# Performance work log

Measured on AMD Instinct MI355X. Metric: run time of the kernel, lower is better.

The kernel has to match this reference:

```python
import jax, jax.numpy as jnp
import numpy as np

EPS_DIAG = 1e-3  # matches torch.eye(len(A)) * 0.001


def _sqrtm_psd(M):
    # Symmetric PSD matrix square root via eigendecomposition.
    # Equivalent to scipy.linalg.sqrtm(...).real for SPD inputs.
    M = 0.5 * (M + M.T)
    w, v = jnp.linalg.eigh(M)
    w = jnp.clip(w, 0.0)
    return (v * jnp.sqrt(w)) @ v.T


def setup_inputs() -> dict:
    key = jax.random.key(0)
    k1, k2 = jax.random.split(key)
    N, D = 4096, 2048
    z_a = jax.random.normal(k1, (N, D), dtype=jnp.float32)
    z_b = jax.random.normal(k2, (N, D), dtype=jnp.float32)
    return {"z_a": z_a, "z_b": z_b}


def reference(z_a, z_b):
    # norm=True branch: per-feature standardization; torch std uses ddof=1
    n = z_a.shape[0]
    z_a = (z_a - z_a.mean(axis=0)) / (z_a.std(axis=0, ddof=1))
    z_b = (z_b - z_b.mean(axis=0)) / (z_b.std(axis=0, ddof=1))
    A = z_a.T @ z_a  # [D, D]
    B = z_b.T @ z_b  # [D, D]
    D = A.shape[0]
    eps = jnp.eye(D, dtype=A.dtype) * EPS_DIAG
    A = A + eps
    B = B + eps
    B12 = _sqrtm_psd(B)
    C = _sqrtm_psd(B12 @ A @ B12)
    return jnp.trace(A + B - 2.0 * C)
```

## Files before the change

kernel.cpp:

```cpp
#include <hip/hip_runtime.h>
#include <math.h>

typedef unsigned short u16;
typedef unsigned int u32;

#define D_DIM 2048
#define N_ROWS 4096
#define EPS_DIAG 1e-3f
#define NS_ITERS 16

typedef __attribute__((ext_vector_type(8))) short bf16x8;
typedef __attribute__((ext_vector_type(4))) float f32x4;

__device__ __forceinline__ u16 f2bf(float f) {
  u32 u = __float_as_uint(f);
  u += 0x7fffu + ((u >> 16) & 1u);
  return (u16)(u >> 16);
}
__device__ __forceinline__ float bf2f(u16 h) {
  return __uint_as_float(((u32)h) << 16);
}

#define GLD16(g, l)                                        \
  __builtin_amdgcn_global_load_lds(                        \
      (const __attribute__((address_space(1))) void*)(g),  \
      (__attribute__((address_space(3))) void*)(l), 16, 0, 0)



__device__ __forceinline__ void swz256(int id, int& bi, int& bj) {
  int s = id & 7;
  int j = id >> 3;
  bj = s * 2 + (j & 1);
  bi = j >> 1;
}


__global__ __launch_bounds__(256)
void k_colstats2(const float* __restrict__ za, const float* __restrict__ zb,
                 float* __restrict__ stat) {
  const float* z = blockIdx.z ? zb : za;
  float* sum_ = stat + blockIdx.z * 2 * D_DIM;
  float* ssq_ = sum_ + D_DIM;
  const int c = blockIdx.x * 256 + threadIdx.x;
  const int r0 = blockIdx.y * (N_ROWS / 16);
  float s = 0.f, q = 0.f;
#pragma unroll 8
  for (int r = 0; r < N_ROWS / 16; ++r) {
    float v = z[(size_t)(r0 + r) * D_DIM + c];
    s += v;
    q += v * v;
  }
  atomicAdd(&sum_[c], s);
  atomicAdd(&ssq_[c], q);
}

__global__ __launch_bounds__(256)
void k_finalize_stats(float* stat) {
  const int t = blockIdx.x * 256 + threadIdx.x;
  const int g = t >> 11;
  const int c = t & (D_DIM - 1);
  float* base = stat + g * 2 * D_DIM;
  float s = base[c];
  float q = base[D_DIM + c];
  float mean = s * (1.0f / N_ROWS);
  float var = (q - (float)N_ROWS * mean * mean) * (1.0f / (N_ROWS - 1));
  var = fmaxf(var, 1e-30f);
  base[c] = mean;
  base[D_DIM + c] = 1.0f / sqrtf(var);
}


__global__ __launch_bounds__(256)
void k_zsplit_t2(const float* __restrict__ za, const float* __restrict__ zb,
                 const float* __restrict__ stat, u16* __restrict__ Zh0,
                 u16* __restrict__ Zl0, u16* __restrict__ Zh1,
                 u16* __restrict__ Zl1) {
  __shared__ float T[64 * 72];
  const float* z = blockIdx.z ? zb : za;
  const float* mean = stat + blockIdx.z * 2 * D_DIM;
  const float* rstd = mean + D_DIM;
  u16* Zth = blockIdx.z ? Zh1 : Zh0;
  u16* Ztl = blockIdx.z ? Zl1 : Zl0;
  const int t = threadIdx.x;
  const int r0 = blockIdx.x * 64;
  const int c0 = blockIdx.y * 64;
#pragma unroll
  for (int p = 0; p < 4; ++p) {
    int row = p * 16 + (t >> 4);
    int c4 = t & 15;
    float4 v = *(const float4*)(z + (size_t)(r0 + row) * D_DIM + c0 + c4 * 4);
    *(float4*)&T[row * 72 + c4 * 4] = v;
  }
  __syncthreads();
  const int c = c0 + (t >> 2);
  const float m = mean[c];
  const float r = rstd[c];
  const int cc = t >> 2;
#pragma unroll
  for (int g = 0; g < 2; ++g) {
    int rbase = g * 32 + (t & 3) * 8;
    u16 hs[8], ls[8];
#pragma unroll
    for (int i = 0; i < 8; ++i) {
      float x = (T[(rbase + i) * 72 + cc] - m) * r;
      hs[i] = f2bf(x);
      ls[i] = f2bf(x - bf2f(hs[i]));
    }
    uint4 ph, pl;
    ph.x = (u32)hs[0] | ((u32)hs[1] << 16);
    ph.y = (u32)hs[2] | ((u32)hs[3] << 16);
    ph.z = (u32)hs[4] | ((u32)hs[5] << 16);
    ph.w = (u32)hs[6] | ((u32)hs[7] << 16);
    pl.x = (u32)ls[0] | ((u32)ls[1] << 16);
    pl.y = (u32)ls[2] | ((u32)ls[3] << 16);
    pl.z = (u32)ls[4] | ((u32)ls[5] << 16);
    pl.w = (u32)ls[6] | ((u32)ls[7] << 16);
    int n = r0 + rbase;
    int slot = ((n >> 3) & 7) ^ (c & 7);
    size_t o = (size_t)c * N_ROWS + (size_t)((n & ~63) | (slot << 3));
    *(uint4*)(Zth + o) = ph;
    *(uint4*)(Ztl + o) = pl;
  }
}

#define FINVC 1
#define FTRACE 4
#define FCOL 8
#define FROW 16

__device__ __forceinline__ void nn_body(
    u16* lds, const u16* __restrict__ Xh, const u16* __restrict__ Xl,
    const u16* __restrict__ Wh, const u16* __restrict__ Wl,
    u16* __restrict__ Crh, u16* __restrict__ Crl, u16* __restrict__ Cch,
    u16* __restrict__ Ccl, float* __restrict__ scal, int K, float diag,
    float pmul, int flags, int tidx, int bi, int bj) {
  const int tid = threadIdx.x;
  const int lane = tid & 63;
  const int w = tid >> 6;
  const int I = bi * 128;
  const int J = bj * 128;

  size_t xro[4], wro[4];
  int lbase[4];
#pragma unroll
  for (int p = 0; p < 4; ++p) {
    int rl = w * 32 + p * 8;
    xro[p] = (size_t)(I + rl + (lane >> 3)) * K + (lane & 7) * 8;
    wro[p] = (size_t)(J + rl + (lane >> 3)) * K + (lane & 7) * 8;
    lbase[p] = rl * 64;
  }

  f32x4 acc[2][8];
#pragma unroll
  for (int i = 0; i < 2; ++i)
#pragma unroll
    for (int j = 0; j < 8; ++j) acc[i][j] = (f32x4){0.f, 0.f, 0.f, 0.f};

#define NN_STAGE(k1, buf)                                         \
  {                                                               \
    _Pragma("unroll") for (int p = 0; p < 4; ++p) {               \
      GLD16(Xh + xro[p] + (k1), &lds[(buf) + lbase[p]]);          \
      GLD16(Xl + xro[p] + (k1), &lds[(buf) + 8192 + lbase[p]]);   \
      GLD16(Wh + wro[p] + (k1), &lds[(buf) + 16384 + lbase[p]]);  \
      GLD16(Wl + wro[p] + (k1), &lds[(buf) + 24576 + lbase[p]]);  \
    }                                                             \
  }

#define NN_COMPUTE(CUR)                                                   \
  {                                                                       \
    _Pragma("unroll") for (int ks = 0; ks < 2; ++ks) {                    \
      bf16x8 fxh[2], fxl[2];                                              \
      _Pragma("unroll") for (int i = 0; i < 2; ++i) {                     \
        int m = w * 32 + i * 16 + (lane & 15);                            \
        int sl = m * 64 + (((ks * 4 + (lane >> 4)) ^ (m & 7)) << 3);      \
        fxh[i] = *(const bf16x8*)&lds[(CUR) + sl];                        \
        fxl[i] = *(const bf16x8*)&lds[(CUR) + 8192 + sl];                 \
      }                                                                   \
      _Pragma("unroll") for (int jb = 0; jb < 2; ++jb) {                  \
        bf16x8 fwh[4], fwl[4];                                            \
        _Pragma("unroll") for (int jj = 0; jj < 4; ++jj) {                \
          int n = (jb * 4 + jj) * 16 + (lane & 15);                       \
          int sl = n * 64 + (((ks * 4 + (lane >> 4)) ^ (n & 7)) << 3);    \
          fwh[jj] = *(const bf16x8*)&lds[(CUR) + 16384 + sl];             \
          fwl[jj] = *(const bf16x8*)&lds[(CUR) + 24576 + sl];             \
        }                                                                 \
        _Pragma("unroll") for (int i = 0; i < 2; ++i)                     \
          _Pragma("unroll") for (int jj = 0; jj < 4; ++jj) {              \
            acc[i][jb * 4 + jj] = __builtin_amdgcn_mfma_f32_16x16x32_bf16(\
                fxh[i], fwh[jj], acc[i][jb * 4 + jj], 0, 0, 0);           \
            acc[i][jb * 4 + jj] = __builtin_amdgcn_mfma_f32_16x16x32_bf16(\
                fxh[i], fwl[jj], acc[i][jb * 4 + jj], 0, 0, 0);           \
            acc[i][jb * 4 + jj] = __builtin_amdgcn_mfma_f32_16x16x32_bf16(\
                fxl[i], fwh[jj], acc[i][jb * 4 + jj], 0, 0, 0);           \
          }                                                               \
      }                                                                   \
    }                                                                     \
  }

  const int nk = K >> 6;
  NN_STAGE(0, 0);
  for (int k = 0; k < nk; ++k) {
    const int cur = (k & 1) * 32768;
    const int nxt = 32768 - cur;
    __builtin_amdgcn_s_barrier();
    __builtin_amdgcn_sched_barrier(0);
    if (k + 1 < nk) {
      NN_STAGE((k + 1) * 64, nxt);
      __builtin_amdgcn_sched_barrier(0);
      asm volatile("s_waitcnt vmcnt(16)" ::: "memory");
    } else {
      asm volatile("s_waitcnt vmcnt(0)" ::: "memory");
    }
    __builtin_amdgcn_s_barrier();
    __builtin_amdgcn_sched_barrier(0);
    NN_COMPUTE(cur);
  }
  __syncthreads();
#undef NN_COMPUTE
#undef NN_STAGE

  const int qd = lane >> 4;
  const int nl = lane & 15;
  float pm = pmul;
  if (flags & FINVC) pm = pmul / scal[5];

#define NN_VAL(i, j, r, out)                           \
  {                                                    \
    int gi_ = I + w * 32 + (i)*16 + qd * 4 + (r);      \
    int gj_ = J + (j)*16 + nl;                         \
    out = pm * acc[i][j][r];                           \
    if (gi_ == gj_) out += diag;                       \
  }

  if (flags & FTRACE) {
    float ts = 0.f;
#pragma unroll
    for (int i = 0; i < 2; ++i)
#pragma unroll
      for (int j = 0; j < 8; ++j)
#pragma unroll
        for (int r = 0; r < 4; ++r) {
          int gi = I + w * 32 + i * 16 + qd * 4 + r;
          int gj = J + j * 16 + nl;
          if (gi == gj) {
            float v;
            NN_VAL(i, j, r, v);
            ts += v;
          }
        }
#pragma unroll
    for (int o = 32; o > 0; o >>= 1) ts += __shfl_down(ts, o, 64);
    float* red = (float*)lds;
    if (lane == 0) red[w] = ts;
    __syncthreads();
    if (tid == 0) atomicAdd(&scal[tidx], red[0] + red[1] + red[2] + red[3]);
    __syncthreads();
  }

  const int wbp = w * 4352;
  for (int half = 0; half < 2; ++half) {
#pragma unroll
    for (int i = 0; i < 2; ++i)
#pragma unroll
      for (int j = 0; j < 8; ++j)
#pragma unroll
        for (int r = 0; r < 4; ++r) {
          float v;
          NN_VAL(i, j, r, v);
          u16 hv = f2bf(v);
          u16 sv = half ? f2bf(v - bf2f(hv)) : hv;
          lds[wbp + (i * 16 + qd * 4 + r) * 136 + j * 16 + nl] = sv;
        }
    __syncthreads();
    if (flags & FROW) {
      u16* dst = half ? Crl : Crh;
#pragma unroll
      for (int p2 = 0; p2 < 8; ++p2) {
        int rr = lane >> 1;
        int ch = (lane & 1) + p2 * 2;
        bf16x8 vv = *(const bf16x8*)&lds[wbp + rr * 136 + ch * 8];
        int gi = I + w * 32 + rr;
        int slot = (ch & 7) ^ (gi & 7);
        size_t o = (size_t)gi * D_DIM + J + ((ch >> 3) << 6) + (slot << 3);
        *(bf16x8*)(dst + o) = vv;
      }
    }
    if (flags & FCOL) {
      u16* dst = half ? Ccl : Cch;
#pragma unroll
      for (int jj = 0; jj < 8; ++jj) {
        int cmaj = J + jj * 16 + (lane >> 2);
        int run = (lane & 3) * 8;
        int m = I + w * 32 + run;
        u16 tp[8];
#pragma unroll
        for (int r2 = 0; r2 < 8; ++r2) tp[r2] = lds[wbp + (run + r2) * 136 +
                                                    jj * 16 + (lane >> 2)];
        uint4 pk;
        pk.x = (u32)tp[0] | ((u32)tp[1] << 16);
        pk.y = (u32)tp[2] | ((u32)tp[3] << 16);
        pk.z = (u32)tp[4] | ((u32)tp[5] << 16);
        pk.w = (u32)tp[6] | ((u32)tp[7] << 16);
        int slot = ((m >> 3) & 7) ^ (cmaj & 7);
        size_t o = (size_t)cmaj * D_DIM + (m & ~63) + (slot << 3);
        *(uint4*)(dst + o) = pk;
      }
    }
    __syncthreads();
  }
#undef NN_VAL
}

__global__ __launch_bounds__(256)
void k_nn(const u16* Xh, const u16* Xl, const u16* Wh, const u16* Wl, u16* Crh,
          u16* Crl, u16* Cch, u16* Ccl, float* scal, int K, float diag,
          float pmul, int flags, int tidx) {
  __shared__ u16 lds[65536];
  int bi, bj;
  swz256(blockIdx.x + (blockIdx.y << 4), bi, bj);
  nn_body(lds, Xh, Xl, Wh, Wl, Crh, Crl, Cch, Ccl, scal, K, diag, pmul, flags,
          tidx, bi, bj);
}

__global__ __launch_bounds__(256)
void k_nn_tri2(const u16* Xh0, const u16* Xl0, u16* Ch0, u16* Cl0,
               const u16* Xh1, const u16* Xl1, u16* Ch1, u16* Cl1,
               float* scal) {
  __shared__ u16 lds[65536];
  int x = blockIdx.x;
  int f5 = (x & 7) * 34 + (x >> 3);
  int g = (f5 >= 136) ? 1 : 0;
  int f = f5 - g * 136;
  int bi = (int)((sqrtf(8.f * (float)f + 1.f) - 1.f) * 0.5f);
  while (bi * (bi + 1) / 2 > f) --bi;
  while ((bi + 1) * (bi + 2) / 2 <= f) ++bi;
  int bj = f - bi * (bi + 1) / 2;
  if (g)
    nn_body(lds, Xh1, Xl1, Xh1, Xl1, Ch1, Cl1, Ch1, Cl1, scal, N_ROWS,
            EPS_DIAG, 1.0f, FROW | FCOL | FTRACE, 2, bi, bj);
  else
    nn_body(lds, Xh0, Xl0, Xh0, Xl0, Ch0, Cl0, Ch0, Cl0, scal, N_ROWS,
            EPS_DIAG, 1.0f, FROW | FCOL | FTRACE, 1, bi, bj);
}

struct NN2Args {
  const u16 *xh0, *xl0, *wh0, *wl0;
  u16 *crh0, *crl0, *cch0, *ccl0;
  const u16 *xh1, *xl1, *wh1, *wl1;
  u16 *crh1, *crl1, *cch1, *ccl1;
  float pm0, pm1;
};

__global__ __launch_bounds__(256)
void k_nn2(NN2Args a, float* scal) {
  __shared__ u16 lds[65536];
  int bi, bj;
  swz256(blockIdx.x + (blockIdx.y << 4), bi, bj);
  if (blockIdx.z == 0)
    nn_body(lds, a.xh0, a.xl0, a.wh0, a.wl0, a.crh0, a.crl0, a.cch0, a.ccl0,
            scal, D_DIM, 0.f, a.pm0, FROW | FCOL, 0, bi, bj);
  else
    nn_body(lds, a.xh1, a.xl1, a.wh1, a.wl1, a.crh1, a.crl1, a.cch1, a.ccl1,
            scal, D_DIM, 0.f, a.pm1, FROW | FCOL, 0, bi, bj);
}


__global__ __launch_bounds__(256)
void k_pones2(float* __restrict__ va, float* __restrict__ vb,
              float* __restrict__ snA, float* __restrict__ snB) {
  int t = blockIdx.x * 256 + threadIdx.x;
  if (t < D_DIM)
    va[t] = 1.0f;
  else
    vb[t - D_DIM] = 1.0f;
  if (t == 0) {
    snA[0] = 1.0f;
    snB[0] = 1.0f;
  }
}

__global__ __launch_bounds__(256)
void k_gemv2(const u16* __restrict__ Ah, const u16* __restrict__ Bh,
             const float* viA, float* voA, const float* viB, float* voB,
             const float* snA, const float* snB, u32* smA, u32* smB) {
  const int zc = blockIdx.y;
  const u16* Mh = zc ? Bh : Ah;
  const float* vin = zc ? viB : viA;
  float* vout = zc ? voB : voA;
  const float* snorm = zc ? snB : snA;
  u32* smax = zc ? smB : smA;
  __shared__ float vs[D_DIM];
  float inv = 1.0f / snorm[0];
  for (int i = threadIdx.x; i < D_DIM; i += 256) vs[i] = vin[i] * inv;
  __syncthreads();
  int row = blockIdx.x * 4 + (threadIdx.x >> 6);
  int lane = threadIdx.x & 63;
  const u16* r = Mh + (size_t)row * D_DIM;
  float s = 0.f;
  for (int c0 = lane * 8; c0 < D_DIM; c0 += 512) {
    int k0 = (c0 & ~63) | ((((c0 >> 3) & 7) ^ (row & 7)) << 3);
    uint4 p = *(const uint4*)(r + c0);
    u32 w4[4] = {p.x, p.y, p.z, p.w};
#pragma unroll
    for (int q = 0; q < 4; ++q) {
      s += bf2f((u16)(w4[q] & 0xffff)) * vs[k0 + 2 * q];
      s += bf2f((u16)(w4[q] >> 16)) * vs[k0 + 2 * q + 1];
    }
  }
#pragma unroll
  for (int o = 32; o > 0; o >>= 1) s += __shfl_down(s, o, 64);
  if (lane == 0) {
    vout[row] = s;
    atomicMax(smax, __float_as_uint(fabsf(s)));
  }
}

__global__ void k_setc(float* scal) {
  scal[5] = 1.1f * scal[11] * scal[21];
}

__global__ __launch_bounds__(256)
void k_t1(const u16* __restrict__ Mrh, const u16* __restrict__ Mrl,
          const u16* __restrict__ Mth, const u16* __restrict__ Mtl,
          const float* __restrict__ scal, u16* __restrict__ Trh,
          u16* __restrict__ Trl, u16* __restrict__ Tth, u16* __restrict__ Ttl) {
  size_t t = (size_t)blockIdx.x * 256 + threadIdx.x;
  float invc = 1.0f / scal[5];
  size_t e = t * 4;
  int i = (int)(e >> 11);
  int u0 = (int)(e & (D_DIM - 1));
  int jb = (u0 & ~63) | ((((u0 >> 3) & 7) ^ (i & 7)) << 3) | (u0 & 7);
#pragma unroll
  for (int pass = 0; pass < 2; ++pass) {
    const u16* sh = pass ? Mth : Mrh;
    const u16* sl = pass ? Mtl : Mrl;
    u16* dh = pass ? Tth : Trh;
    u16* dl = pass ? Ttl : Trl;
    uint2 hv = ((const uint2*)sh)[t];
    uint2 lv = ((const uint2*)sl)[t];
    u16 hs[4] = {(u16)(hv.x & 0xffff), (u16)(hv.x >> 16), (u16)(hv.y & 0xffff),
                 (u16)(hv.y >> 16)};
    u16 ls[4] = {(u16)(lv.x & 0xffff), (u16)(lv.x >> 16), (u16)(lv.y & 0xffff),
                 (u16)(lv.y >> 16)};
    u16 th[4], tl[4];
#pragma unroll
    for (int c = 0; c < 4; ++c) {
      float m = bf2f(hs[c]) + bf2f(ls[c]);
      float tv = ((i == jb + c) ? 3.0f : 0.0f) - m * invc;
      th[c] = f2bf(tv);
      tl[c] = f2bf(tv - bf2f(th[c]));
    }
    ((uint2*)dh)[t] = make_uint2((u32)th[0] | ((u32)th[1] << 16),
                                 (u32)th[2] | ((u32)th[3] << 16));
    ((uint2*)dl)[t] = make_uint2((u32)tl[0] | ((u32)tl[1] << 16),
                                 (u32)tl[2] | ((u32)tl[3] << 16));
  }
}

__global__ __launch_bounds__(256)
void k_trdot(const u16* __restrict__ Ah, const u16* __restrict__ Al,
             const u16* __restrict__ Bh, const u16* __restrict__ Bl,
             double* __restrict__ acc) {
  size_t t = (size_t)blockIdx.x * 256 + threadIdx.x;
  uint2 ah = ((const uint2*)Ah)[t], al = ((const uint2*)Al)[t];
  uint2 bh = ((const uint2*)Bh)[t], bl = ((const uint2*)Bl)[t];
  float s = 0.f;
  u32 ha[4] = {ah.x & 0xffffu, ah.x >> 16, ah.y & 0xffffu, ah.y >> 16};
  u32 la[4] = {al.x & 0xffffu, al.x >> 16, al.y & 0xffffu, al.y >> 16};
  u32 hb[4] = {bh.x & 0xffffu, bh.x >> 16, bh.y & 0xffffu, bh.y >> 16};
  u32 lb[4] = {bl.x & 0xffffu, bl.x >> 16, bl.y & 0xffffu, bl.y >> 16};
#pragma unroll
  for (int c = 0; c < 4; ++c)
    s += (bf2f((u16)ha[c]) + bf2f((u16)la[c])) *
         (bf2f((u16)hb[c]) + bf2f((u16)lb[c]));
#pragma unroll
  for (int o = 32; o > 0; o >>= 1) s += __shfl_down(s, o, 64);
  __shared__ float red[4];
  if ((threadIdx.x & 63) == 0) red[threadIdx.x >> 6] = s;
  __syncthreads();
  if (threadIdx.x == 0)
    atomicAdd(acc, (double)(red[0] + red[1] + red[2] + red[3]));
}

__global__ void k_final2(const float* __restrict__ scal,
                         const double* __restrict__ dot,
                         float* __restrict__ out) {
  out[0] = scal[1] + scal[2] - sqrtf(scal[5]) * (float)dot[0];
}


__global__ __launch_bounds__(256)
void k_zsplit(const float* __restrict__ z, const float* __restrict__ mean,
              const float* __restrict__ rstd, u16* __restrict__ zh,
              u16* __restrict__ zl) {
  size_t t = (size_t)blockIdx.x * 256 + threadIdx.x;
  int ci = (int)(t & 511);
  float4 v = ((const float4*)z)[t];
  float4 m = ((const float4*)mean)[ci];
  float4 r = ((const float4*)rstd)[ci];
  float x[4] = {(v.x - m.x) * r.x, (v.y - m.y) * r.y, (v.z - m.z) * r.z,
                (v.w - m.w) * r.w};
  u16 h[4], l[4];
#pragma unroll
  for (int i = 0; i < 4; ++i) {
    h[i] = f2bf(x[i]);
    l[i] = f2bf(x[i] - bf2f(h[i]));
  }
  ((uint2*)zh)[t] = make_uint2((u32)h[0] | ((u32)h[1] << 16),
                               (u32)h[2] | ((u32)h[3] << 16));
  ((uint2*)zl)[t] = make_uint2((u32)l[0] | ((u32)l[1] << 16),
                               (u32)l[2] | ((u32)l[3] << 16));
}

__global__ __launch_bounds__(256)
void k_gram_mm(const u16* __restrict__ zh, const u16* __restrict__ zl,
               u16* __restrict__ Oh, u16* __restrict__ Ol) {
  __shared__ u16 lds[24576];
  const int tid = threadIdx.x;
  const int lane = tid & 63;
  const int w = tid >> 6;
  const int I = blockIdx.y * 128;
  const int J = blockIdx.x * 64;
  const int kp = tid >> 4;
  const int nc = tid & 15;
  const int qq = kp >> 2;
  const int kd = (kp & 3) * 2;
  const size_t aro = (size_t)(2 * kp) * D_DIM + I + nc * 8;
  const size_t bro = (size_t)(2 * kp) * D_DIM + J + nc * 4;
  union U4 { uint4 v; u16 s[8]; };
  union U2 { uint2 v; u16 s[4]; };
  U4 ah0, ah1, al0, al1;
  U2 bh0, bh1, bl0, bl1;
  f32x4 acc[2][4];
#pragma unroll
  for (int i = 0; i < 2; ++i)
#pragma unroll
    for (int j = 0; j < 4; ++j) acc[i][j] = (f32x4){0.f, 0.f, 0.f, 0.f};
#define GRAM_LOAD(k1)                         \
  {                                           \
    size_t ao = aro + (size_t)(k1)*D_DIM;     \
    size_t bo = bro + (size_t)(k1)*D_DIM;     \
    ah0.v = *(const uint4*)(zh + ao);         \
    ah1.v = *(const uint4*)(zh + ao + D_DIM); \
    al0.v = *(const uint4*)(zl + ao);         \
    al1.v = *(const uint4*)(zl + ao + D_DIM); \
    bh0.v = *(const uint2*)(zh + bo);         \
    bh1.v = *(const uint2*)(zh + bo + D_DIM); \
    bl0.v = *(const uint2*)(zl + bo);         \
    bl1.v = *(const uint2*)(zl + bo + D_DIM); \
  }
#define GRAM_PACK(buf)                                                       \
  {                                                                          \
    _Pragma("unroll") for (int j = 0; j < 8; ++j) {                          \
      int mc = nc * 8 + j;                                                   \
      int t2 = mc >> 4, ml = mc & 15;                                        \
      int slot = (t2 * 64 + qq * 16 + ml) ^ t2;                              \
      *(u32*)&lds[(buf) + slot * 8 + kd] =                                   \
          (u32)ah0.s[j] | ((u32)ah1.s[j] << 16);                             \
      *(u32*)&lds[(buf) + 4096 + slot * 8 + kd] =                            \
          (u32)al0.s[j] | ((u32)al1.s[j] << 16);                             \
    }                                                                        \
    _Pragma("unroll") for (int j = 0; j < 4; ++j) {                          \
      int n = nc * 4 + j;                                                    \
      int u = n >> 4, nl = n & 15;                                           \
      int slot = (u * 64 + qq * 16 + nl) ^ u;                                \
      *(u32*)&lds[(buf) + 8192 + slot * 8 + kd] =                            \
          (u32)bh0.s[j] | ((u32)bh1.s[j] << 16);                             \
      *(u32*)&lds[(buf) + 10240 + slot * 8 + kd] =                           \
          (u32)bl0.s[j] | ((u32)bl1.s[j] << 16);                             \
    }                                                                        \
  }
  GRAM_LOAD(0);
  GRAM_PACK(0);
  __syncthreads();
  for (int k = 0; k < N_ROWS / 32; ++k) {
    const int cur = (k & 1) * 12288;
    const int nxt = 12288 - cur;
    if (k < N_ROWS / 32 - 1) GRAM_LOAD((k + 1) * 32);
    bf16x8 fah[2], fal[2], fbh[4], fbl[4];
#pragma unroll
    for (int i = 0; i < 2; ++i) {
      int t2 = w * 2 + i;
      int sl = (t2 * 64 + lane) ^ t2;
      fah[i] = *(const bf16x8*)&lds[cur + sl * 8];
      fal[i] = *(const bf16x8*)&lds[cur + 4096 + sl * 8];
    }
#pragma unroll
    for (int j = 0; j < 4; ++j) {
      int sl = (j * 64 + lane) ^ j;
      fbh[j] = *(const bf16x8*)&lds[cur + 8192 + sl * 8];
      fbl[j] = *(const bf16x8*)&lds[cur + 10240 + sl * 8];
    }
#pragma unroll
    for (int i = 0; i < 2; ++i)
#pragma unroll
      for (int j = 0; j < 4; ++j) {
        acc[i][j] = __builtin_amdgcn_mfma_f32_16x16x32_bf16(fah[i], fbh[j],
                                                            acc[i][j], 0, 0, 0);
        acc[i][j] = __builtin_amdgcn_mfma_f32_16x16x32_bf16(fah[i], fbl[j],
                                                            acc[i][j], 0, 0, 0);
        acc[i][j] = __builtin_amdgcn_mfma_f32_16x16x32_bf16(fal[i], fbh[j],
                                                            acc[i][j], 0, 0, 0);
      }
    if (k < N_ROWS / 32 - 1) GRAM_PACK(nxt);
    __syncthreads();
  }
  const int qd = lane >> 4;
  const int nl = lane & 15;
#pragma unroll
  for (int i = 0; i < 2; ++i)
#pragma unroll
    for (int j = 0; j < 4; ++j)
#pragma unroll
      for (int r = 0; r < 4; ++r) {
        int gi = I + w * 32 + i * 16 + qd * 4 + r;
        int gj = J + j * 16 + nl;
        float v = acc[i][j][r] + ((gi == gj) ? EPS_DIAG : 0.f);
        u16 h = f2bf(v);
        u16 l = f2bf(v - bf2f(h));
        Oh[(size_t)gi * D_DIM + gj] = h;
        Ol[(size_t)gi * D_DIM + gj] = l;
      }
#undef GRAM_LOAD
#undef GRAM_PACK
}

template <int MODE>
__global__ __launch_bounds__(256)
void k_mm(const u16* __restrict__ Ph, const u16* __restrict__ Pl,
          const u16* __restrict__ Qh, const u16* __restrict__ Ql,
          u16* __restrict__ Ch, u16* __restrict__ Cl,
          const float* __restrict__ scal) {
  __shared__ u16 lds[24576];
  const int tid = threadIdx.x;
  const int lane = tid & 63;
  const int w = tid >> 6;
  const int I = blockIdx.y * 128;
  const int J = blockIdx.x * 64;
  const int kp = tid >> 4;
  const int nc = tid & 15;
  const int qq = kp >> 2;
  const int kd = (kp & 3) * 2;
  size_t aro[2];
  int acl[2], abase[2];
#pragma unroll
  for (int p = 0; p < 2; ++p) {
    int s = p * 256 + w * 64 + lane;
    aro[p] = (size_t)(I + (s >> 6) * 16 + (s & 15)) * D_DIM;
    acl[p] = ((s >> 4) & 3) * 8;
    abase[p] = (p * 256 + w * 64) * 8;
  }
  const size_t bro = (size_t)(2 * kp) * D_DIM + J + nc * 4;
  union U2 { uint2 v; u16 s[4]; };
  U2 bh0, bh1, bl0, bl1;
  f32x4 acc[2][4];
#pragma unroll
  for (int i = 0; i < 2; ++i)
#pragma unroll
    for (int j = 0; j < 4; ++j) acc[i][j] = (f32x4){0.f, 0.f, 0.f, 0.f};
#define MM_STAGE_A(k1, buf)                                              \
  {                                                                      \
    _Pragma("unroll") for (int p = 0; p < 2; ++p) {                      \
      GLD16(Ph + aro[p] + (k1) + acl[p], &lds[(buf) + abase[p]]);        \
      GLD16(Pl + aro[p] + (k1) + acl[p], &lds[(buf) + 4096 + abase[p]]); \
    }                                                                    \
  }
#define MM_LOAD_B(k1)                         \
  {                                           \
    size_t bo = bro + (size_t)(k1)*D_DIM;     \
    bh0.v = *(const uint2*)(Qh + bo);         \
    bh1.v = *(const uint2*)(Qh + bo + D_DIM); \
    bl0.v = *(const uint2*)(Ql + bo);         \
    bl1.v = *(const uint2*)(Ql + bo + D_DIM); \
  }
#define MM_PACK_B(buf)                                                       \
  {                                                                          \
    _Pragma("unroll") for (int j = 0; j < 4; ++j) {                          \
      int n = nc * 4 + j;                                                    \
      int u = n >> 4, nl2 = n & 15;                                          \
      int slot = (u * 64 + qq * 16 + nl2) ^ u;                               \
      *(u32*)&lds[(buf) + 8192 + slot * 8 + kd] =                            \
          (u32)bh0.s[j] | ((u32)bh1.s[j] << 16);                             \
      *(u32*)&lds[(buf) + 10240 + slot * 8 + kd] =                           \
          (u32)bl0.s[j] | ((u32)bl1.s[j] << 16);                             \
    }                                                                        \
  }
  MM_STAGE_A(0, 0);
  MM_LOAD_B(0);
  MM_PACK_B(0);
  __syncthreads();
  for (int k = 0; k < D_DIM / 32; ++k) {
    const int cur = (k & 1) * 12288;
    const int nxt = 12288 - cur;
    if (k < D_DIM / 32 - 1) {
      MM_STAGE_A((k + 1) * 32, nxt);
      MM_LOAD_B((k + 1) * 32);
    }
    bf16x8 fah[2], fal[2], fbh[4], fbl[4];
#pragma unroll
    for (int i = 0; i < 2; ++i) {
      int t2 = w * 2 + i;
      fah[i] = *(const bf16x8*)&lds[cur + (t2 * 64 + lane) * 8];
      fal[i] = *(const bf16x8*)&lds[cur + 4096 + (t2 * 64 + lane) * 8];
    }
#pragma unroll
    for (int j = 0; j < 4; ++j) {
      int sl = (j * 64 + lane) ^ j;
      fbh[j] = *(const bf16x8*)&lds[cur + 8192 + sl * 8];
      fbl[j] = *(const bf16x8*)&lds[cur + 10240 + sl * 8];
    }
#pragma unroll
    for (int i = 0; i < 2; ++i)
#pragma unroll
      for (int j = 0; j < 4; ++j) {
        acc[i][j] = __builtin_amdgcn_mfma_f32_16x16x32_bf16(fah[i], fbh[j],
                                                            acc[i][j], 0, 0, 0);
        acc[i][j] = __builtin_amdgcn_mfma_f32_16x16x32_bf16(fah[i], fbl[j],
                                                            acc[i][j], 0, 0, 0);
        acc[i][j] = __builtin_amdgcn_mfma_f32_16x16x32_bf16(fal[i], fbh[j],
                                                            acc[i][j], 0, 0, 0);
      }
    if (k < D_DIM / 32 - 1) MM_PACK_B(nxt);
    __syncthreads();
  }
  float mul = (MODE == 2) ? 0.5f : 1.0f;
  if (MODE == 3) mul = 0.5f / sqrtf(scal[0]);
  const int qd = lane >> 4;
  const int nl = lane & 15;
#pragma unroll
  for (int i = 0; i < 2; ++i)
#pragma unroll
    for (int j = 0; j < 4; ++j)
#pragma unroll
      for (int r = 0; r < 4; ++r) {
        int gi = I + w * 32 + i * 16 + qd * 4 + r;
        int gj = J + j * 16 + nl;
        float v = acc[i][j][r];
        if (MODE == 1)
          v = ((gi == gj) ? 3.0f : 0.0f) - v;
        else
          v *= mul;
        u16 h = f2bf(v);
        u16 l = f2bf(v - bf2f(h));
        Ch[(size_t)gi * D_DIM + gj] = h;
        Cl[(size_t)gi * D_DIM + gj] = l;
      }
#undef MM_STAGE_A
#undef MM_LOAD_B
#undef MM_PACK_B
}

__global__ __launch_bounds__(256)
void k_frob_hl(const u16* __restrict__ mh, const u16* __restrict__ ml,
               float* __restrict__ c2) {
  size_t t = (size_t)blockIdx.x * 256 + threadIdx.x;
  uint2 hv = ((const uint2*)mh)[t];
  uint2 lv = ((const uint2*)ml)[t];
  float v0 = bf2f((u16)(hv.x & 0xffff)) + bf2f((u16)(lv.x & 0xffff));
  float v1 = bf2f((u16)(hv.x >> 16)) + bf2f((u16)(lv.x >> 16));
  float v2 = bf2f((u16)(hv.y & 0xffff)) + bf2f((u16)(lv.y & 0xffff));
  float v3 = bf2f((u16)(hv.y >> 16)) + bf2f((u16)(lv.y >> 16));
  float q = v0 * v0 + v1 * v1 + v2 * v2 + v3 * v3;
#pragma unroll
  for (int o = 32; o > 0; o >>= 1) q += __shfl_down(q, o, 64);
  __shared__ float red[4];
  if ((threadIdx.x & 63) == 0) red[threadIdx.x >> 6] = q;
  __syncthreads();
  if (threadIdx.x == 0) atomicAdd(c2, red[0] + red[1] + red[2] + red[3]);
}

__global__ __launch_bounds__(256)
void k_t1z1(const u16* __restrict__ Mh, const u16* __restrict__ Ml,
            const float* __restrict__ scal, u16* __restrict__ Th,
            u16* __restrict__ Tl, u16* __restrict__ Zh, u16* __restrict__ Zl) {
  size_t t = (size_t)blockIdx.x * 256 + threadIdx.x;
  float invc = 1.0f / sqrtf(scal[0]);
  size_t e = t * 4;
  int i = (int)(e >> 11);
  int j0 = (int)(e & (D_DIM - 1));
  uint2 hv = ((const uint2*)Mh)[t];
  uint2 lv = ((const uint2*)Ml)[t];
  u16 hs[4] = {(u16)(hv.x & 0xffff), (u16)(hv.x >> 16), (u16)(hv.y & 0xffff),
               (u16)(hv.y >> 16)};
  u16 ls[4] = {(u16)(lv.x & 0xffff), (u16)(lv.x >> 16), (u16)(lv.y & 0xffff),
               (u16)(lv.y >> 16)};
  u16 th[4], tl[4], zh[4], zl[4];
#pragma unroll
  for (int c = 0; c < 4; ++c) {
    float m = bf2f(hs[c]) + bf2f(ls[c]);
    float tv = ((i == j0 + c) ? 3.0f : 0.0f) - m * invc;
    th[c] = f2bf(tv);
    tl[c] = f2bf(tv - bf2f(th[c]));
    float zv = 0.5f * tv;
    zh[c] = f2bf(zv);
    zl[c] = f2bf(zv - bf2f(zh[c]));
  }
  ((uint2*)Th)[t] = make_uint2((u32)th[0] | ((u32)th[1] << 16),
                               (u32)th[2] | ((u32)th[3] << 16));
  ((uint2*)Tl)[t] = make_uint2((u32)tl[0] | ((u32)tl[1] << 16),
                               (u32)tl[2] | ((u32)tl[3] << 16));
  ((uint2*)Zh)[t] = make_uint2((u32)zh[0] | ((u32)zh[1] << 16),
                               (u32)zh[2] | ((u32)zh[3] << 16));
  ((uint2*)Zl)[t] = make_uint2((u32)zl[0] | ((u32)zl[1] << 16),
                               (u32)zl[2] | ((u32)zl[3] << 16));
}

__global__ __launch_bounds__(256)
void k_trace_hl(const u16* __restrict__ mh, const u16* __restrict__ ml,
                float* __restrict__ out) {
  __shared__ float red[256];
  float s = 0.f;
  for (int i = threadIdx.x; i < D_DIM; i += 256) {
    size_t d = (size_t)i * (D_DIM + 1);
    s += bf2f(mh[d]) + bf2f(ml[d]);
  }
  red[threadIdx.x] = s;
  __syncthreads();
  for (int o = 128; o > 0; o >>= 1) {
    if (threadIdx.x < o) red[threadIdx.x] += red[threadIdx.x + o];
    __syncthreads();
  }
  if (threadIdx.x == 0) out[0] = red[0];
}

__global__ __launch_bounds__(256)
void k_final(const u16* __restrict__ Yh, const u16* __restrict__ Yl,
             const float* __restrict__ scal, float* __restrict__ out) {
  __shared__ float red[256];
  float s = 0.f;
  for (int i = threadIdx.x; i < D_DIM; i += 256) {
    size_t d = (size_t)i * (D_DIM + 1);
    s += bf2f(Yh[d]) + bf2f(Yl[d]);
  }
  red[threadIdx.x] = s;
  __syncthreads();
  for (int o = 128; o > 0; o >>= 1) {
    if (threadIdx.x < o) red[threadIdx.x] += red[threadIdx.x + o];
    __syncthreads();
  }
  if (threadIdx.x == 0) {
    float sqrtc = sqrtf(sqrtf(scal[0]));
    out[0] = scal[1] + scal[2] - 2.0f * sqrtc * red[0];
  }
}


extern "C" void kernel_launch(void* const* d_in, const int* in_sizes, int n_in,
                              void* d_out, int out_size, void* d_ws,
                              size_t ws_size, hipStream_t stream) {
  (void)in_sizes; (void)n_in; (void)out_size;
  const float* za = (const float*)d_in[0];
  const float* zb = (const float*)d_in[1];
  float* out = (float*)d_out;
  float* ws = (float*)d_ws;
  float* stat = ws;
  float* scal = ws + 4 * D_DIM;

  hipMemsetAsync(ws, 0, (4 * D_DIM + 32) * sizeof(float), stream);
  dim3 blk(256);

  const size_t NEED = 65536ull + 8ull * 16 * 1024 * 1024;
  if (ws_size >= NEED) {
    char* pool = (char*)d_ws + 65536;
    auto uh = [&](int u) { return (u16*)(pool + (size_t)u * 16777216); };
    auto ul = [&](int u) {
      return (u16*)(pool + (size_t)u * 16777216 + 8388608);
    };
    u16* ZhA = (u16*)(pool);
    u16* ZlA = (u16*)(pool + 1ull * 16777216);
    u16* ZhB = (u16*)(pool + 4ull * 16777216);
    u16* ZlB = (u16*)(pool + 5ull * 16777216);
    dim3 gm(16, 16);

    k_colstats2<<<dim3(8, 16, 2), blk, 0, stream>>>(za, zb, stat);
    k_finalize_stats<<<16, blk, 0, stream>>>(stat);
    k_zsplit_t2<<<dim3(64, 32, 2), blk, 0, stream>>>(za, zb, stat, ZhA, ZlA,
                                                     ZhB, ZlB);
    k_nn_tri2<<<272, blk, 0, stream>>>(ZhA, ZlA, uh(2), ul(2), ZhB, ZlB,
                                       uh(3), ul(3), scal);

    k_pones2<<<16, blk, 0, stream>>>(stat, stat + 2 * D_DIM, scal + 6,
                                     scal + 16);
    for (int s = 0; s < 5; ++s) {
      const float* viA = (s & 1) ? stat + D_DIM : stat;
      float* voA = (s & 1) ? stat : stat + D_DIM;
      const float* viB = (s & 1) ? stat + 3 * D_DIM : stat + 2 * D_DIM;
      float* voB = (s & 1) ? stat + 2 * D_DIM : stat + 3 * D_DIM;
      k_gemv2<<<dim3(512, 2), blk, 0, stream>>>(
          uh(2), uh(3), viA, voA, viB, voB, scal + 6 + s, scal + 16 + s,
          (u32*)(scal + 7 + s), (u32*)(scal + 17 + s));
    }
    k_setc<<<1, 1, 0, stream>>>(scal);

    k_nn<<<gm, blk, 0, stream>>>(uh(2), ul(2), uh(3), ul(3), uh(4), ul(4),
                                 uh(5), ul(5), scal, D_DIM, 0.f, 1.0f,
                                 FROW | FCOL, 0);
    k_t1<<<4096, blk, 0, stream>>>(uh(4), ul(4), uh(5), ul(5), scal, uh(6),
                                   ul(6), uh(7), ul(7));
    k_nn<<<gm, blk, 0, stream>>>(uh(4), ul(4), uh(7), ul(7), uh(0), ul(0),
                                 uh(1), ul(1), scal, D_DIM, 0.f, 0.5f,
                                 FROW | FCOL | FINVC, 0);
    k_nn<<<gm, blk, 0, stream>>>(uh(6), ul(6), uh(1), ul(1), uh(4), ul(4),
                                 uh(5), ul(5), scal, D_DIM, 3.f, -0.5f,
                                 FROW | FCOL, 0);
    {
      NN2Args a;
      a.xh0 = uh(0); a.xl0 = ul(0); a.wh0 = uh(5); a.wl0 = ul(5);
      a.crh0 = uh(1); a.crl0 = ul(1); a.cch0 = uh(2); a.ccl0 = ul(2);
      a.pm0 = 0.5f;
      a.xh1 = uh(4); a.xl1 = ul(4); a.wh1 = uh(7); a.wl1 = ul(7);
      a.crh1 = uh(3); a.crl1 = ul(3); a.cch1 = uh(6); a.ccl1 = ul(6);
      a.pm1 = 0.25f;
      k_nn2<<<dim3(16, 16, 2), blk, 0, stream>>>(a, scal);
    }
    int Yr = 1, Yt = 2, Zr = 3, Zt = 6;
    int fr0 = 0, fr1 = 4, fr2 = 5, fr3 = 7;
    for (int it = 3; it <= 10; ++it) {
      k_nn<<<gm, blk, 0, stream>>>(uh(Zr), ul(Zr), uh(Yt), ul(Yt), uh(fr0),
                                   ul(fr0), uh(fr1), ul(fr1), scal, D_DIM, 3.f,
                                   -1.f, FROW | FCOL, 0);
      NN2Args a;
      a.xh0 = uh(Yr); a.xl0 = ul(Yr); a.wh0 = uh(fr1); a.wl0 = ul(fr1);
      a.crh0 = uh(fr2); a.crl0 = ul(fr2); a.cch0 = uh(fr3); a.ccl0 = ul(fr3);
      a.pm0 = 0.5f;
      a.xh1 = uh(fr0); a.xl1 = ul(fr0); a.wh1 = uh(Zt); a.wl1 = ul(Zt);
      a.crh1 = uh(Yt); a.crl1 = ul(Yt); a.cch1 = uh(Zr); a.ccl1 = ul(Zr);
      a.pm1 = 0.5f;
      k_nn2<<<dim3(16, 16, 2), blk, 0, stream>>>(a, scal);
      int nYr = fr2, nYt = fr3, nZr = Yt, nZt = Zr;
      int nf0 = Yr, nf1 = Zt, nf2 = fr0, nf3 = fr1;
      Yr = nYr; Yt = nYt; Zr = nZr; Zt = nZt;
      fr0 = nf0; fr1 = nf1; fr2 = nf2; fr3 = nf3;
    }
    k_nn<<<gm, blk, 0, stream>>>(uh(Zr), ul(Zr), uh(Yt), ul(Yt), uh(fr1),
                                 ul(fr1), uh(fr0), ul(fr0), scal, D_DIM, 3.f,
                                 -1.f, FCOL, 0);
    k_trdot<<<4096, blk, 0, stream>>>(uh(Yr), ul(Yr), uh(fr0), ul(fr0),
                                      (double*)(scal + 24));
    k_final2<<<1, 1, 0, stream>>>(scal, (const double*)(scal + 24), out);
    return;
  }

  k_colstats2<<<dim3(8, 16, 2), blk, 0, stream>>>(za, zb, stat);
  k_finalize_stats<<<16, blk, 0, stream>>>(stat);
  u16* b[8];
  {
    char* pool = (char*)d_ws + 65536;
    for (int i = 0; i < 8; ++i) b[i] = (u16*)(pool + (size_t)i * 8388608);
  }
#define PH(p) b[2 * (p)]
#define PL(p) b[2 * (p) + 1]
  u16* zh = b[4];
  u16* zl = b[6];
  dim3 gm(32, 16);
  k_zsplit<<<8192, blk, 0, stream>>>(za, stat, stat + D_DIM, zh, zl);
  k_gram_mm<<<gm, blk, 0, stream>>>(zh, zl, PH(0), PL(0));
  k_zsplit<<<8192, blk, 0, stream>>>(zb, stat + 2 * D_DIM, stat + 3 * D_DIM,
                                     zh, zl);
  k_gram_mm<<<gm, blk, 0, stream>>>(zh, zl, PH(1), PL(1));
  k_trace_hl<<<1, blk, 0, stream>>>(PH(0), PL(0), scal + 1);
  k_trace_hl<<<1, blk, 0, stream>>>(PH(1), PL(1), scal + 2);
  k_mm<0><<<gm, blk, 0, stream>>>(PH(0), PL(0), PH(1), PL(1), PH(2), PL(2),
                                  scal);
  k_frob_hl<<<4096, blk, 0, stream>>>(PH(2), PL(2), scal);
  k_t1z1<<<4096, blk, 0, stream>>>(PH(2), PL(2), scal, PH(0), PL(0), PH(1),
                                   PL(1));
  k_mm<3><<<gm, blk, 0, stream>>>(PH(2), PL(2), PH(0), PL(0), PH(3), PL(3),
                                  scal);
  int Y = 3, Z = 1, fA = 0, fB = 2;
  for (int it = 2; it <= NS_ITERS; ++it) {
    k_mm<1><<<gm, blk, 0, stream>>>(PH(Z), PL(Z), PH(Y), PL(Y), PH(fA), PL(fA),
                                    scal);
    k_mm<2><<<gm, blk, 0, stream>>>(PH(Y), PL(Y), PH(fA), PL(fA), PH(fB),
                                    PL(fB), scal);
    if (it < NS_ITERS)
      k_mm<2><<<gm, blk, 0, stream>>>(PH(fA), PL(fA), PH(Z), PL(Z), PH(Y),
                                      PL(Y), scal);
    int oy = Y, oz = Z, oa = fA, ob = fB;
    Y = ob; Z = oy; fA = oz; fB = oa;
  }
  k_final<<<1, blk, 0, stream>>>(PH(Y), PL(Y), scal, out);
#undef PH
#undef PL
}
```

Before: 2.415 ms.

## Store bf16 matrices in contiguous 8x64 tiles for coalesced LDS staging loads

Changes the global storage layout of the bf16 hi/lo matrices from row-major (swizzled within 64-column chunks) to blocked 8-row by 64-column tiles of 512 contiguous elements. Each wavefront's global_load_lds for an 8-row strip now reads one contiguous 1 KiB span instead of eight strided 128-byte pieces, which should improve memory coalescing in the GEMM. Every producer and consumer (standardize transpose, GEMM row/col epilogues, GEMV, elementwise T kernel) is updated to the new indexing. The risk is a missed consumer in the unseen code that still assumes the old layout.

```diff
diff --git a/kernel.cpp b/kernel.cpp
--- a/kernel.cpp
+++ b/kernel.cpp
@@ -118,7 +118,8 @@
     pl.w = (u32)ls[6] | ((u32)ls[7] << 16);
     int n = r0 + rbase;
     int slot = ((n >> 3) & 7) ^ (c & 7);
-    size_t o = (size_t)c * N_ROWS + (size_t)((n & ~63) | (slot << 3));
+    size_t o = ((size_t)(c >> 3) * (N_ROWS >> 6) + (n >> 6)) * 512 +
+               (c & 7) * 64 + (slot << 3);
     *(uint4*)(Zth + o) = ph;
     *(uint4*)(Ztl + o) = pl;
   }
@@ -146,8 +147,8 @@
 #pragma unroll
   for (int p = 0; p < 4; ++p) {
     int rl = w * 32 + p * 8;
-    xro[p] = (size_t)(I + rl + (lane >> 3)) * K + (lane & 7) * 8;
-    wro[p] = (size_t)(J + rl + (lane >> 3)) * K + (lane & 7) * 8;
+    xro[p] = (size_t)(I + rl) * K + lane * 8;
+    wro[p] = (size_t)(J + rl) * K + lane * 8;
     lbase[p] = rl * 64;
   }
 
@@ -157,14 +158,17 @@
 #pragma unroll
     for (int j = 0; j < 8; ++j) acc[i][j] = (f32x4){0.f, 0.f, 0.f, 0.f};
 
-#define NN_STAGE(k1, buf)                                         \
-  {                                                               \
-    _Pragma("unroll") for (int p = 0; p < 4; ++p) {               \
-      GLD16(Xh + xro[p] + (k1), &lds[(buf) + lbase[p]]);          \
-      GLD16(Xl + xro[p] + (k1), &lds[(buf) + 8192 + lbase[p]]);   \
-      GLD16(Wh + wro[p] + (k1), &lds[(buf) + 16384 + lbase[p]]);  \
-      GLD16(Wl + wro[p] + (k1), &lds[(buf) + 24576 + lbase[p]]);  \
-    }                                                             \
+#define NN_STAGE(k1, buf)                                                  \
+  {                                                                        \
+    _Pragma("unroll") for (int p = 0; p < 4; ++p) {                        \
+      GLD16(Xh + xro[p] + (size_t)(k1) * 8, &lds[(buf) + lbase[p]]);       \
+      GLD16(Xl + xro[p] + (size_t)(k1) * 8,                                \
+            &lds[(buf) + 8192 + lbase[p]]);                                \
+      GLD16(Wh + wro[p] + (size_t)(k1) * 8,                                \
+            &lds[(buf) + 16384 + lbase[p]]);                               \
+      GLD16(Wl + wro[p] + (size_t)(k1) * 8,                                \
+            &lds[(buf) + 24576 + lbase[p]]);                               \
+    }                                                                      \
   }
 
 #define NN_COMPUTE(CUR)                                                   \
@@ -281,8 +285,9 @@
         int ch = (lane & 1) + p2 * 2;
         bf16x8 vv = *(const bf16x8*)&lds[wbp + rr * 136 + ch * 8];
         int gi = I + w * 32 + rr;
-        int slot = (ch & 7) ^ (gi & 7);
-        size_t o = (size_t)gi * D_DIM + J + ((ch >> 3) << 6) + (slot << 3);
+        size_t o = ((size_t)(gi >> 3) * (D_DIM >> 6) + (J >> 6) + (ch >> 3)) *
+                       512 +
+                   (gi & 7) * 64 + (((ch & 7) ^ (gi & 7)) << 3);
         *(bf16x8*)(dst + o) = vv;
       }
     }
@@ -302,8 +307,8 @@
         pk.y = (u32)tp[2] | ((u32)tp[3] << 16);
         pk.z = (u32)tp[4] | ((u32)tp[5] << 16);
         pk.w = (u32)tp[6] | ((u32)tp[7] << 16);
-        int slot = ((m >> 3) & 7) ^ (cmaj & 7);
-        size_t o = (size_t)cmaj * D_DIM + (m & ~63) + (slot << 3);
+        size_t o = ((size_t)(cmaj >> 3) * (D_DIM >> 6) + (m >> 6)) * 512 +
+                   (cmaj & 7) * 64 + ((((m >> 3) & 7) ^ (cmaj & 7)) << 3);
         *(uint4*)(dst + o) = pk;
       }
     }
@@ -396,16 +401,18 @@
   __syncthreads();
   int row = blockIdx.x * 4 + (threadIdx.x >> 6);
   int lane = threadIdx.x & 63;
-  const u16* r = Mh + (size_t)row * D_DIM;
+  const size_t rb = (size_t)(row >> 3) * (D_DIM >> 6);
+  const int rsub = (row & 7) * 64;
   float s = 0.f;
   for (int c0 = lane * 8; c0 < D_DIM; c0 += 512) {
-    int k0 = (c0 & ~63) | ((((c0 >> 3) & 7) ^ (row & 7)) << 3);
-    uint4 p = *(const uint4*)(r + c0);
+    size_t addr = (rb + (c0 >> 6)) * 512 + rsub +
+                  ((((c0 >> 3) & 7) ^ (row & 7)) << 3);
+    uint4 p = *(const uint4*)(Mh + addr);
     u32 w4[4] = {p.x, p.y, p.z, p.w};
 #pragma unroll
     for (int q = 0; q < 4; ++q) {
-      s += bf2f((u16)(w4[q] & 0xffff)) * vs[k0 + 2 * q];
-      s += bf2f((u16)(w4[q] >> 16)) * vs[k0 + 2 * q + 1];
+      s += bf2f((u16)(w4[q] & 0xffff)) * vs[c0 + 2 * q];
+      s += bf2f((u16)(w4[q] >> 16)) * vs[c0 + 2 * q + 1];
     }
   }
 #pragma unroll
@@ -428,9 +435,12 @@
   size_t t = (size_t)blockIdx.x * 256 + threadIdx.x;
   float invc = 1.0f / scal[5];
   size_t e = t * 4;
-  int i = (int)(e >> 11);
-  int u0 = (int)(e & (D_DIM - 1));
-  int jb = (u0 & ~63) | ((((u0 >> 3) & 7) ^ (i & 7)) << 3) | (u0 & 7);
+  int tile = (int)(e >> 9);
+  int within = (int)(e & 511);
+  int rl = within >> 6;
+  int slot = (within >> 3) & 7;
+  int i = (tile / (D_DIM >> 6)) * 8 + rl;
+  int jb = (tile % (D_DIM >> 6)) * 64 + ((slot ^ rl) << 3) + (within & 7);
 #pragma unroll
   for (int pass = 0; pass < 2; ++pass) {
     const u16* sh = pass ? Mth : Mrh;
```

After: 2.391 ms. Within noise of the previous version (-1.0%).
